# Optimization experiments

Hardware: AMD Instinct MI355X
Metric: run time of the kernel (lower is better)

The kernel has to match this reference:

```python
import jax, jax.numpy as jnp
import numpy as np

H = 16          # num_attention_heads
DH = 64         # attention_head_size
HID = H * DH    # hidden_size = 1024
EPS = 1e-12


def _layernorm(x, gamma, beta):
    mu = jnp.mean(x, axis=-1, keepdims=True)
    var = jnp.mean(jnp.square(x - mu), axis=-1, keepdims=True)
    return (x - mu) * jax.lax.rsqrt(var + EPS) * gamma + beta


def _attention(q, k, v, mask, Wo, bo, gamma, beta):
    # q,k,v: [B,S,HID] already linearly projected
    B, Tq, _ = q.shape
    Tk = k.shape[1]
    qh = q.reshape(B, Tq, H, DH)
    kh = k.reshape(B, Tk, H, DH)
    vh = v.reshape(B, Tk, H, DH)
    scores = jnp.einsum('bqhd,bkhd->bhqk', qh, kh) / np.sqrt(DH).astype(q.dtype)
    if mask is not None:
        scores = scores + mask  # mask broadcasts [B,1,1,Tk]
    probs = jax.nn.softmax(scores, axis=-1)
    ctx = jnp.einsum('bhqk,bkhd->bqhd', probs, vh)
    proj = jnp.einsum('bqhd,hdo->bqo', ctx, Wo) + bo
    # NOTE: residual is the projected query q (faithful to the source)
    return _layernorm(q + proj, gamma, beta)


def setup_inputs() -> dict:
    key = jax.random.key(0)
    ks = jax.random.split(key, 20)
    B, T, S = 4, 1024, 1024
    s = 0.02
    inp = {
        'encoder_states': jax.random.normal(ks[0], (B, S, HID), jnp.float32),
        'decoder_inputs': jax.random.normal(ks[1], (B, T, HID), jnp.float32),
        'src_attention_mask': jnp.zeros((B, 1, 1, S), jnp.float32),
        'tgt_attention_mask': jnp.zeros((B, 1, 1, T), jnp.float32),
        'Wq': jax.random.normal(ks[2], (HID, HID), jnp.float32) * s,
        'bq': jnp.zeros((HID,), jnp.float32),
        'Wk': jax.random.normal(ks[3], (HID, HID), jnp.float32) * s,
        'bk': jnp.zeros((HID,), jnp.float32),
        'Wv': jax.random.normal(ks[4], (HID, HID), jnp.float32) * s,
        'bv': jnp.zeros((HID,), jnp.float32),
        'Wq2': jax.random.normal(ks[5], (HID, HID), jnp.float32) * s,
        'bq2': jnp.zeros((HID,), jnp.float32),
        'Wk2': jax.random.normal(ks[6], (HID, HID), jnp.float32) * s,
        'bk2': jnp.zeros((HID,), jnp.float32),
        'Wv2': jax.random.normal(ks[7], (HID, HID), jnp.float32) * s,
        'bv2': jnp.zeros((HID,), jnp.float32),
        'Wo': jax.random.normal(ks[8], (H, DH, HID), jnp.float32) * s,
        'bo': jnp.zeros((HID,), jnp.float32),
        'gamma': jnp.ones((HID,), jnp.float32),
        'beta': jnp.zeros((HID,), jnp.float32),
    }
    return inp


def reference(encoder_states, decoder_inputs, src_attention_mask, tgt_attention_mask,
              Wq, bq, Wk, bk, Wv, bv, Wq2, bq2, Wk2, bk2, Wv2, bv2,
              Wo, bo, gamma, beta):
    # self-attention over decoder inputs
    q1 = decoder_inputs @ Wq + bq
    k1 = decoder_inputs @ Wk + bk
    v1 = decoder_inputs @ Wv + bv
    self_out = _attention(q1, k1, v1, tgt_attention_mask, Wo, bo, gamma, beta)
    # cross-attention: query from self_out, key/value from encoder states
    q2 = self_out @ Wq2 + bq2
    k2 = encoder_states @ Wk2 + bk2
    v2 = encoder_states @ Wv2 + bv2
    return _attention(q2, k2, v2, src_attention_mask, Wo, bo, gamma, beta)
```

## Files before the change

kernel.cpp:

```cpp
#include <hip/hip_runtime.h>
#include <stdint.h>


typedef unsigned short u16;
typedef __bf16 bf16x8 __attribute__((ext_vector_type(8)));
typedef float f32x4 __attribute__((ext_vector_type(4)));

#define AS1 __attribute__((address_space(1)))
#define AS3 __attribute__((address_space(3)))
typedef AS3 char lds_char;
typedef AS3 unsigned short lds_u16;

#define VMCNT(n) asm volatile("s_waitcnt vmcnt(" #n ")" ::: "memory")
#define LGKM0() asm volatile("s_waitcnt lgkmcnt(0)" ::: "memory")
#define SBARRIER() asm volatile("s_barrier" ::: "memory")

__device__ __forceinline__ u16 f2bf(float f) {
  union { float f; uint32_t u; } v; v.f = f;
  uint32_t u = v.u;
  return (u16)((u + 0x7fffu + ((u >> 16) & 1u)) >> 16);
}

__device__ __forceinline__ float bf2f(u16 b) {
  union { uint32_t u; float f; } v; v.u = ((uint32_t)b) << 16;
  return v.f;
}

__device__ __forceinline__ uint32_t cvt_pk_bf16(float lo, float hi) {
  uint32_t r;
  asm("v_cvt_pk_bf16_f32 %0, %1, %2" : "=v"(r) : "v"(lo), "v"(hi));
  return r;
}

__device__ __forceinline__ void gl_lds16(const void* g, void* l) {
  __builtin_amdgcn_global_load_lds((AS1 void*)(g), (AS3 void*)(l), 16, 0, 0);
}

__device__ __forceinline__ bf16x8 dsr128(const lds_u16* p) {
  bf16x8 r;
  asm volatile("ds_read_b128 %0, %1" : "=v"(r) : "v"(p));
  return r;
}

__device__ __forceinline__ int swz(int row, int byte) {
  return row * 128 + (byte ^ ((row & 7) << 4));
}

__global__ void __launch_bounds__(256)
convert2_kernel(const float* __restrict__ in0, u16* __restrict__ out0,
                const float* __restrict__ in1, u16* __restrict__ out1) {
  const int half = blockIdx.x >> 12;
  const int i = (blockIdx.x & 4095) * 256 + threadIdx.x;
  const float* in = half ? in1 : in0;
  u16* out = half ? out1 : out0;
  float4 v = ((const float4*)in)[i];
  ushort4 o;
  o.x = f2bf(v.x); o.y = f2bf(v.y); o.z = f2bf(v.z); o.w = f2bf(v.w);
  ((ushort4*)out)[i] = o;
}

struct WP { const float* w[7]; };

__global__ void __launch_bounds__(256)
transpose_kernel(WP wp, u16* __restrict__ out) {
  __shared__ float tile[64][65];
  const float* W = wp.w[blockIdx.z];
  u16* Wt = out + (size_t)blockIdx.z * 1024 * 1024;
  const int k0 = blockIdx.y * 64, n0 = blockIdx.x * 64;
  const int t = threadIdx.x;
  const int r = t >> 4, c4 = (t & 15) * 4;
#pragma unroll
  for (int rr = 0; rr < 64; rr += 16) {
    float4 v = *(const float4*)&W[(size_t)(k0 + r + rr) * 1024 + n0 + c4];
    tile[r + rr][c4 + 0] = v.x; tile[r + rr][c4 + 1] = v.y;
    tile[r + rr][c4 + 2] = v.z; tile[r + rr][c4 + 3] = v.w;
  }
  __syncthreads();
  const int n = t >> 2, seg = (t & 3) * 16;
  union { u16 s[16]; uint4 q[2]; } u;
#pragma unroll
  for (int i = 0; i < 16; ++i) u.s[i] = f2bf(tile[seg + i][n]);
  uint4* dst = (uint4*)&Wt[(size_t)(n0 + n) * 1024 + k0 + seg];
  dst[0] = u.q[0]; dst[1] = u.q[1];
}

__global__ void __launch_bounds__(512, 2)
qkv4c_kernel(const u16* __restrict__ A0, const u16* __restrict__ A1,
             const u16* __restrict__ A2, const u16* __restrict__ Bt,
             const float* __restrict__ b0, const float* __restrict__ b1,
             const float* __restrict__ b2,
             u16* __restrict__ qb, u16* __restrict__ kb, u16* __restrict__ vt) {
  __shared__ u16 SH[65536];

  const int d = blockIdx.y * 12 + blockIdx.x;
  const int c = d & 7, ci = d >> 3;
  const int mt = (c & 3) * 4 + (ci & 3);
  const int nt = (c >> 2) * 6 + (ci >> 2);
  const int bm = mt * 256, bn = nt * 256;
  const int seg = nt >> 2;
  const u16* A = (seg == 0) ? A0 : (seg == 1) ? A1 : A2;

  const int t = threadIdx.x, wv = t >> 6, ln = t & 63;
  const int wm = (wv >> 2) * 128, wn = (wv & 3) * 64;
  const int lcol = ln & 15, g = ln >> 4;
  const int aoff = (g * 16) ^ (((lcol >> 1) & 3) << 4);

  lds_char* ABase = (lds_char*)&SH[0];
  lds_char* BBase = (lds_char*)&SH[32768];

  const int st_row = wv * 16 + (ln >> 2);
  const int st_srcb = (((ln & 3) ^ ((ln >> 3) & 3)) * 16);
  auto stageA = [&](int buf, int k0) {
#pragma unroll
    for (int hf = 0; hf < 2; ++hf) {
      const int row = hf * 128 + st_row;
      gl_lds16((const char*)A + ((size_t)(bm + row) * 1024 + k0) * 2 + st_srcb,
               (char*)&SH[0] + buf * 16384 + hf * 8192 + wv * 1024);
    }
  };
  auto stageB = [&](int buf, int k0) {
#pragma unroll
    for (int hf = 0; hf < 2; ++hf) {
      const int row = hf * 128 + st_row;
      gl_lds16((const char*)Bt + ((size_t)(bn + row) * 1024 + k0) * 2 + st_srcb,
               (char*)&SH[32768] + buf * 16384 + hf * 8192 + wv * 1024);
    }
  };

  f32x4 acc[8][4] = {};

  stageA(0, 0); stageB(0, 0);
  stageA(1, 32); stageB(1, 32);
  stageA(2, 64); stageB(2, 64);
  VMCNT(8);
  __builtin_amdgcn_s_barrier();

  for (int kt = 0; kt < 32; ++kt) {
    const int buf = kt & 3;
    lds_char* Ab = ABase + buf * 16384;
    lds_char* Bb = BBase + buf * 16384;
    const int sbuf = (kt + 3) & 3;
    const int sk = (kt + 3) * 32;
    const bool do_st = kt < 29;
    bf16x8 afr[4], bfr[4];

#pragma unroll
    for (int j = 0; j < 4; ++j)
      bfr[j] = dsr128((const lds_u16*)(Bb + (wn + j * 16 + lcol) * 64 + aoff));
#pragma unroll
    for (int i = 0; i < 4; ++i)
      afr[i] = dsr128((const lds_u16*)(Ab + (wm + i * 16 + lcol) * 64 + aoff));
    if (do_st) stageA(sbuf, sk);
    __builtin_amdgcn_s_barrier();
    LGKM0();
    __builtin_amdgcn_sched_barrier(0);
    __builtin_amdgcn_s_setprio(1);
#pragma unroll
    for (int i = 0; i < 4; ++i)
#pragma unroll
      for (int j = 0; j < 4; ++j)
        acc[i][j] = __builtin_amdgcn_mfma_f32_16x16x32_bf16(afr[i], bfr[j], acc[i][j], 0, 0, 0);
    __builtin_amdgcn_s_setprio(0);
    __builtin_amdgcn_s_barrier();

#pragma unroll
    for (int i = 0; i < 4; ++i)
      afr[i] = dsr128((const lds_u16*)(Ab + (wm + 64 + i * 16 + lcol) * 64 + aoff));
    if (do_st) stageB(sbuf, sk);
    __builtin_amdgcn_s_barrier();
    LGKM0();
    __builtin_amdgcn_sched_barrier(0);
    __builtin_amdgcn_s_setprio(1);
#pragma unroll
    for (int i = 0; i < 4; ++i)
#pragma unroll
      for (int j = 0; j < 4; ++j)
        acc[4 + i][j] = __builtin_amdgcn_mfma_f32_16x16x32_bf16(afr[i], bfr[j], acc[4 + i][j], 0, 0, 0);
    __builtin_amdgcn_s_setprio(0);
    if (kt < 29)       { VMCNT(8); }
    else if (kt == 29) { VMCNT(4); }
    else if (kt == 30) { VMCNT(0); }
    __builtin_amdgcn_s_barrier();
  }

  const int cs = bn & 1023;
  const float* bias = (seg == 0) ? b0 : (seg == 1) ? b1 : b2;

  if (seg == 2) {
#pragma unroll
    for (int j = 0; j < 4; ++j) {
      const int col_l = wn + j * 16 + lcol;
      const float bc = bias[cs + col_l];
#pragma unroll
      for (int i = 0; i < 8; ++i) {
        const int m4 = wm + i * 16 + g * 4;
        ushort4 o;
        o.x = f2bf(acc[i][j][0] + bc); o.y = f2bf(acc[i][j][1] + bc);
        o.z = f2bf(acc[i][j][2] + bc); o.w = f2bf(acc[i][j][3] + bc);
        *(ushort4*)((char*)SH + col_l * 512 + ((m4 * 2) ^ ((col_l & 7) << 4))) = o;
      }
    }
  } else {
#pragma unroll
    for (int j = 0; j < 4; ++j) {
      const int col_l = wn + j * 16 + lcol;
      const float bc = bias[cs + col_l];
#pragma unroll
      for (int i = 0; i < 8; ++i) {
        const int m0 = wm + i * 16 + g * 4;
#pragma unroll
        for (int r = 0; r < 4; ++r)
          SH[(m0 + r) * 256 + (col_l ^ (((m0 + r) & 7) << 3))] = f2bf(acc[i][j][r] + bc);
      }
    }
  }
  __builtin_amdgcn_s_barrier();

  {
    const int R = t >> 1, hb = t & 1;
    u16* gp;
    if (seg == 2) {
      const int col = cs + R;
      const int h = col >> 6, dd = col & 63;
      gp = vt + ((size_t)((bm >> 10) * 16 + h) * 64 + dd) * 1024 + (bm & 1023) + hb * 128;
    } else {
      u16* outp = (seg == 0) ? qb : kb;
      gp = outp + (size_t)(bm + R) * 1024 + cs + hb * 128;
    }
#pragma unroll
    for (int cix = 0; cix < 16; ++cix) {
      uint4 v = *(uint4*)((char*)SH + R * 512 + ((hb * 256 + cix * 16) ^ ((R & 7) << 4)));
      *(uint4*)(gp + cix * 8) = v;
    }
  }
}

__global__ void __launch_bounds__(256)
gemm_proj(const u16* __restrict__ A, const u16* __restrict__ Bt,
          const float* __restrict__ bias, const u16* __restrict__ resid,
          float* __restrict__ outf) {
  __shared__ u16 Alds[2][8192];
  __shared__ u16 Blds[2][8192];
  const int d = blockIdx.y * 8 + blockIdx.x;
  const int c = d & 7, ci = d >> 3;
  const int mt = (c & 3) * 8 + (ci & 7);
  const int nt = (c >> 2) * 4 + (ci >> 3);
  const int bm = mt * 128, bn = nt * 128;
  const int t = threadIdx.x, wv = t >> 6, ln = t & 63;
  const int wm = (wv >> 1) * 64, wn = (wv & 1) * 64;
  const int lcol = ln & 15, lk8 = (ln >> 4) * 8, lr4 = (ln >> 4) * 4;

  f32x4 acc[4][4] = {};

  auto STAGE = [&](int buf, int k0) {
#pragma unroll
    for (int cc = 0; cc < 4; ++cc) {
      const int o = cc * 4096 + wv * 1024 + ln * 16;
      const int row = o >> 7, colb = o & 127;
      gl_lds16((const char*)A + ((size_t)(bm + row) * 1024 + k0) * 2 + colb,
               (char*)Alds[buf] + cc * 4096 + wv * 1024);
      gl_lds16((const char*)Bt + ((size_t)(bn + row) * 1024 + k0) * 2 + colb,
               (char*)Blds[buf] + cc * 4096 + wv * 1024);
    }
  };

  auto COMPUTE = [&](int buf) {
    const u16* Ab = Alds[buf];
    const u16* Bb = Blds[buf];
#pragma unroll
    for (int ks = 0; ks < 2; ++ks) {
      bf16x8 a[4], b[4];
#pragma unroll
      for (int i = 0; i < 4; ++i)
        a[i] = *(const bf16x8*)&Ab[(wm + i * 16 + lcol) * 64 + ks * 32 + lk8];
#pragma unroll
      for (int j = 0; j < 4; ++j)
        b[j] = *(const bf16x8*)&Bb[(wn + j * 16 + lcol) * 64 + ks * 32 + lk8];
#pragma unroll
      for (int i = 0; i < 4; ++i)
#pragma unroll
        for (int j = 0; j < 4; ++j)
          acc[i][j] = __builtin_amdgcn_mfma_f32_16x16x32_bf16(a[i], b[j], acc[i][j], 0, 0, 0);
    }
  };

  STAGE(0, 0);
  int cur = 0;
  for (int it = 0; it < 15; ++it) {
    STAGE(cur ^ 1, (it + 1) * 64);
    VMCNT(8);
    SBARRIER();
    COMPUTE(cur);
    SBARRIER();
    cur ^= 1;
  }
  VMCNT(0);
  SBARRIER();
  COMPUTE(cur);

#pragma unroll
  for (int j = 0; j < 4; ++j) {
    const int col = bn + wn + j * 16 + lcol;
    const float bc = bias[col];
#pragma unroll
    for (int i = 0; i < 4; ++i) {
      const int row0 = bm + wm + i * 16 + lr4;
#pragma unroll
      for (int r = 0; r < 4; ++r) {
        const size_t idx = (size_t)(row0 + r) * 1024 + col;
        outf[idx] = acc[i][j][r] + bc + bf2f(resid[idx]);
      }
    }
  }
}

__global__ void __launch_bounds__(256)
attn_kernel(const u16* __restrict__ Q, const u16* __restrict__ Kb,
            const u16* __restrict__ Vt, const float* __restrict__ mask,
            u16* __restrict__ ctx) {
  __shared__ u16 Klds[2][64 * 64];
  __shared__ u16 Vlds[2][64 * 64];
  __shared__ u16 Plds[4][16 * 64];

  const int fid = blockIdx.x;
  const int xcd = fid & 7, idx = fid >> 3;
  const int bh = xcd * 8 + (idx >> 4);
  const int b = bh >> 4, h = bh & 15;
  const int q0 = (idx & 15) * 64;

  const int t = threadIdx.x, wv = t >> 6, ln = t & 63;
  const int lcol = ln & 15, g = ln >> 4;
  const int lk8 = g * 8, c0 = g * 16;

  const int qrow = q0 + wv * 16 + lcol;
  const u16* qptr = Q + ((size_t)(b * 1024 + qrow) * 1024 + h * 64);
  bf16x8 qa[2];
  qa[0] = *(const bf16x8*)(qptr + lk8);
  qa[1] = *(const bf16x8*)(qptr + 32 + lk8);

  const float* mrow = mask + b * 1024;
  char* pbase = (char*)&Plds[wv][0];

  f32x4 accO[4] = {};
  float m_r = -1e30f, l_r = 0.f;

  auto STAGE = [&](int buf, int s0) {
#pragma unroll
    for (int c = 0; c < 2; ++c) {
      const int o = c * 4096 + wv * 1024 + ln * 16;
      const int row = o >> 7;
      const int src_cb = (o & 127) ^ ((row & 7) << 4);
      gl_lds16((const char*)Kb + ((size_t)((b * 1024 + s0 + row) * 1024 + h * 64)) * 2 + src_cb,
               (char*)Klds[buf] + c * 4096 + wv * 1024);
      gl_lds16((const char*)Vt + ((size_t)(((b * 16 + h) * 64 + row) * 1024 + s0)) * 2 + src_cb,
               (char*)Vlds[buf] + c * 4096 + wv * 1024);
    }
  };

  auto TILE = [&](int buf, const float4* mk) {
    f32x4 accST[4] = {};
    __builtin_amdgcn_s_setprio(1);
#pragma unroll
    for (int ks = 0; ks < 2; ++ks)
#pragma unroll
      for (int sb = 0; sb < 4; ++sb) {
        bf16x8 kb = *(const bf16x8*)((const char*)Klds[buf] + swz(sb * 16 + lcol, ks * 64 + c0));
        accST[sb] = __builtin_amdgcn_mfma_f32_16x16x32_bf16(kb, qa[ks], accST[sb], 0, 0, 0);
      }
    __builtin_amdgcn_s_setprio(0);

    float sv[4][4];
#pragma unroll
    for (int sb = 0; sb < 4; ++sb) {
      sv[sb][0] = accST[sb][0] * 0.125f + mk[sb].x;
      sv[sb][1] = accST[sb][1] * 0.125f + mk[sb].y;
      sv[sb][2] = accST[sb][2] * 0.125f + mk[sb].z;
      sv[sb][3] = accST[sb][3] * 0.125f + mk[sb].w;
    }
    float mt = sv[0][0];
#pragma unroll
    for (int sb = 0; sb < 4; ++sb)
#pragma unroll
      for (int r = 0; r < 4; ++r) mt = fmaxf(mt, sv[sb][r]);
    mt = fmaxf(mt, __shfl_xor(mt, 16));
    mt = fmaxf(mt, __shfl_xor(mt, 32));

    const bool nr = __all(mt <= m_r + 8.0f) != 0;
    float alpha = 1.0f;
    if (!nr) {
      const float mn2 = fmaxf(m_r, mt);
      alpha = __expf(m_r - mn2);
      m_r = mn2;
    }
    float rs = 0.f;
#pragma unroll
    for (int sb = 0; sb < 4; ++sb)
#pragma unroll
      for (int r = 0; r < 4; ++r) {
        const float pp = __expf(sv[sb][r] - m_r);
        sv[sb][r] = pp;
        rs += pp;
      }
    rs += __shfl_xor(rs, 16);
    rs += __shfl_xor(rs, 32);
    l_r = nr ? (l_r + rs) : (l_r * alpha + rs);

#pragma unroll
    for (int sb = 0; sb < 4; ++sb) {
      uint2 dd;
      dd.x = cvt_pk_bf16(sv[sb][0], sv[sb][1]);
      dd.y = cvt_pk_bf16(sv[sb][2], sv[sb][3]);
      *(uint2*)(pbase + swz(lcol, sb * 32 + g * 8)) = dd;
    }

    if (!nr) {
#pragma unroll
      for (int df = 0; df < 4; ++df)
#pragma unroll
        for (int r = 0; r < 4; ++r) accO[df][r] *= alpha;
    }
    __builtin_amdgcn_s_setprio(1);
#pragma unroll
    for (int ks = 0; ks < 2; ++ks) {
      bf16x8 pb = *(const bf16x8*)(pbase + swz(lcol, ks * 64 + c0));
#pragma unroll
      for (int df = 0; df < 4; ++df) {
        bf16x8 va = *(const bf16x8*)((const char*)Vlds[buf] + swz(df * 16 + lcol, ks * 64 + c0));
        accO[df] = __builtin_amdgcn_mfma_f32_16x16x32_bf16(va, pb, accO[df], 0, 0, 0);
      }
    }
    __builtin_amdgcn_s_setprio(0);
  };

  STAGE(0, 0);
  float4 mk_cur[4];
#pragma unroll
  for (int sb = 0; sb < 4; ++sb)
    mk_cur[sb] = *(const float4*)&mrow[sb * 16 + g * 4];

  int cur = 0;
  for (int ti = 0; ti < 15; ++ti) {
    const int s1 = ti * 64 + 64;
    STAGE(cur ^ 1, s1);
    float4 mk_nxt[4];
#pragma unroll
    for (int sb = 0; sb < 4; ++sb)
      mk_nxt[sb] = *(const float4*)&mrow[s1 + sb * 16 + g * 4];
    VMCNT(12);
    SBARRIER();
    TILE(cur, mk_cur);
    SBARRIER();
#pragma unroll
    for (int sb = 0; sb < 4; ++sb) mk_cur[sb] = mk_nxt[sb];
    cur ^= 1;
  }
  VMCNT(4);
  SBARRIER();
  TILE(cur, mk_cur);

  const float inv = 1.0f / l_r;
  u16* cp = ctx + ((size_t)(b * 1024 + qrow) * 1024 + h * 64);
#pragma unroll
  for (int df = 0; df < 4; ++df) {
    ushort4 o;
    o.x = f2bf(accO[df][0] * inv); o.y = f2bf(accO[df][1] * inv);
    o.z = f2bf(accO[df][2] * inv); o.w = f2bf(accO[df][3] * inv);
    *(ushort4*)(cp + df * 16 + g * 4) = o;
  }
}

template <int OUTF>
__global__ void __launch_bounds__(256)
ln_kernel(const float* __restrict__ x, const float* __restrict__ gamma,
          const float* __restrict__ beta, float* __restrict__ outf,
          u16* __restrict__ outb) {
  const int row = blockIdx.x, t = threadIdx.x;
  const float* xr = x + (size_t)row * 1024;
  float4 v = *(const float4*)&xr[t * 4];
  float s = v.x + v.y + v.z + v.w;
  float q = v.x * v.x + v.y * v.y + v.z * v.z + v.w * v.w;
#pragma unroll
  for (int off = 1; off < 64; off <<= 1) {
    s += __shfl_xor(s, off);
    q += __shfl_xor(q, off);
  }
  __shared__ float ws[4], wq[4];
  if ((t & 63) == 0) { ws[t >> 6] = s; wq[t >> 6] = q; }
  __syncthreads();
  s = ws[0] + ws[1] + ws[2] + ws[3];
  q = wq[0] + wq[1] + wq[2] + wq[3];
  const float mu = s * (1.0f / 1024.0f);
  float var = q * (1.0f / 1024.0f) - mu * mu;
  var = fmaxf(var, 0.0f);
  const float rstd = rsqrtf(var + 1e-12f);
  float4 g = *(const float4*)&gamma[t * 4];
  float4 be = *(const float4*)&beta[t * 4];
  float y0 = (v.x - mu) * rstd * g.x + be.x;
  float y1 = (v.y - mu) * rstd * g.y + be.y;
  float y2 = (v.z - mu) * rstd * g.z + be.z;
  float y3 = (v.w - mu) * rstd * g.w + be.w;
  if constexpr (OUTF) {
    float4 o; o.x = y0; o.y = y1; o.z = y2; o.w = y3;
    *(float4*)&outf[(size_t)row * 1024 + t * 4] = o;
  } else {
    ushort4 o; o.x = f2bf(y0); o.y = f2bf(y1); o.z = f2bf(y2); o.w = f2bf(y3);
    *(ushort4*)&outb[(size_t)row * 1024 + t * 4] = o;
  }
}

extern "C" void kernel_launch(void* const* d_in, const int* in_sizes, int n_in,
                              void* d_out, int out_size, void* d_ws, size_t ws_size,
                              hipStream_t stream) {
  const float* enc = (const float*)d_in[0];
  const float* dec = (const float*)d_in[1];
  const float* src_mask = (const float*)d_in[2];
  const float* tgt_mask = (const float*)d_in[3];
  const float* Wq  = (const float*)d_in[4];  const float* bq  = (const float*)d_in[5];
  const float* Wk  = (const float*)d_in[6];  const float* bk  = (const float*)d_in[7];
  const float* Wv  = (const float*)d_in[8];  const float* bv  = (const float*)d_in[9];
  const float* Wq2 = (const float*)d_in[10]; const float* bq2 = (const float*)d_in[11];
  const float* Wk2 = (const float*)d_in[12]; const float* bk2 = (const float*)d_in[13];
  const float* Wv2 = (const float*)d_in[14]; const float* bv2 = (const float*)d_in[15];
  const float* Wo  = (const float*)d_in[16]; const float* bo  = (const float*)d_in[17];
  const float* gamma = (const float*)d_in[18]; const float* beta = (const float*)d_in[19];
  float* out = (float*)d_out;

  char* p = (char*)d_ws;
  const size_t ABF = (size_t)4096 * 1024 * 2;
  const size_t AF  = (size_t)4096 * 1024 * 4;
  const size_t WBF = (size_t)1024 * 1024 * 2;
  u16* decbf = (u16*)p; p += ABF;
  u16* encbf = (u16*)p; p += ABF;
  u16* wt    = (u16*)p; p += 7 * WBF;
  u16* qbf   = (u16*)p; p += ABF;
  u16* kbf   = (u16*)p; p += ABF;
  u16* vtb   = (u16*)p; p += ABF;
  u16* ctxb  = (u16*)p; p += ABF;
  float* tmpf = (float*)p; p += AF;
  u16* sobf  = decbf;

  u16* WoT  = wt + 6 * 1048576;

  dim3 b256(256);
  convert2_kernel<<<8192, b256, 0, stream>>>(dec, decbf, enc, encbf);
  WP wp;
  wp.w[0] = Wq; wp.w[1] = Wk; wp.w[2] = Wv; wp.w[3] = Wq2;
  wp.w[4] = Wk2; wp.w[5] = Wv2; wp.w[6] = Wo;
  transpose_kernel<<<dim3(16, 16, 7), b256, 0, stream>>>(wp, wt);

  qkv4c_kernel<<<dim3(12, 16), 512, 0, stream>>>(
      decbf, decbf, decbf, wt, bq, bk, bv, qbf, kbf, vtb);
  attn_kernel<<<1024, b256, 0, stream>>>(qbf, kbf, vtb, tgt_mask, ctxb);
  gemm_proj<<<dim3(8, 32), b256, 0, stream>>>(ctxb, WoT, bo, qbf, tmpf);
  ln_kernel<0><<<4096, b256, 0, stream>>>(tmpf, gamma, beta, nullptr, sobf);
  qkv4c_kernel<<<dim3(12, 16), 512, 0, stream>>>(
      sobf, encbf, encbf, wt + 3 * 1048576, bq2, bk2, bv2, qbf, kbf, vtb);
  attn_kernel<<<1024, b256, 0, stream>>>(qbf, kbf, vtb, src_mask, ctxb);
  gemm_proj<<<dim3(8, 32), b256, 0, stream>>>(ctxb, WoT, bo, qbf, tmpf);
  ln_kernel<1><<<4096, b256, 0, stream>>>(tmpf, gamma, beta, out, nullptr);
}
```

Before: 233.9 us.

## Shrink QKV GEMM tiles to 256x128 and triple-buffer swizzled projection GEMM

The fused QKV GEMM moves from 256x256 tiles with four LDS buffers to 256x128 tiles with three buffers, smaller LDS and a higher occupancy hint. The grid doubles to 384 blocks to fill more CUs. The output projection GEMM gets a three-stage pipeline with XOR-swizzled LDS layout, full 64-wide K per iteration and priority hints, aiming to cut bank conflicts and hide load latency. Smaller tiles lower data reuse per block and add global traffic in exchange for better parallelism.

```diff
diff --git a/kernel.cpp b/kernel.cpp
--- a/kernel.cpp
+++ b/kernel.cpp
@@ -84,73 +84,62 @@
   dst[0] = u.q[0]; dst[1] = u.q[1];
 }
 
-__global__ void __launch_bounds__(512, 2)
-qkv4c_kernel(const u16* __restrict__ A0, const u16* __restrict__ A1,
+__global__ void __launch_bounds__(512, 4)
+qkv3b_kernel(const u16* __restrict__ A0, const u16* __restrict__ A1,
              const u16* __restrict__ A2, const u16* __restrict__ Bt,
              const float* __restrict__ b0, const float* __restrict__ b1,
              const float* __restrict__ b2,
              u16* __restrict__ qb, u16* __restrict__ kb, u16* __restrict__ vt) {
-  __shared__ u16 SH[65536];
-
-  const int d = blockIdx.y * 12 + blockIdx.x;
+  __shared__ u16 SH[36864];
+
+  const int d = blockIdx.y * 24 + blockIdx.x;
   const int c = d & 7, ci = d >> 3;
-  const int mt = (c & 3) * 4 + (ci & 3);
-  const int nt = (c >> 2) * 6 + (ci >> 2);
-  const int bm = mt * 256, bn = nt * 256;
-  const int seg = nt >> 2;
+  const int mt = ci & 15, nt = c * 3 + (ci >> 4);
+  const int bm = mt * 256, bn = nt * 128;
+  const int seg = nt >> 3;
+  const int cs = (nt & 7) * 128;
   const u16* A = (seg == 0) ? A0 : (seg == 1) ? A1 : A2;
 
   const int t = threadIdx.x, wv = t >> 6, ln = t & 63;
-  const int wm = (wv >> 2) * 128, wn = (wv & 3) * 64;
+  const int wm = (wv >> 1) * 64, wn = (wv & 1) * 64;
   const int lcol = ln & 15, g = ln >> 4;
   const int aoff = (g * 16) ^ (((lcol >> 1) & 3) << 4);
 
-  lds_char* ABase = (lds_char*)&SH[0];
-  lds_char* BBase = (lds_char*)&SH[32768];
-
-  const int st_row = wv * 16 + (ln >> 2);
-  const int st_srcb = (((ln & 3) ^ ((ln >> 3) & 3)) * 16);
-  auto stageA = [&](int buf, int k0) {
-#pragma unroll
-    for (int hf = 0; hf < 2; ++hf) {
-      const int row = hf * 128 + st_row;
+  lds_char* base = (lds_char*)&SH[0];
+  const int st_srcb = (((t & 3) ^ ((t >> 3) & 3)) * 16);
+  auto STAGE = [&](int buf, int k0) {
+#pragma unroll
+    for (int l = 0; l < 2; ++l) {
+      const int row = l * 128 + (t >> 2);
       gl_lds16((const char*)A + ((size_t)(bm + row) * 1024 + k0) * 2 + st_srcb,
-               (char*)&SH[0] + buf * 16384 + hf * 8192 + wv * 1024);
+               (char*)base + buf * 24576 + l * 8192 + (t >> 6) * 1024);
+    }
+    {
+      const int row = t >> 2;
+      gl_lds16((const char*)Bt + ((size_t)(bn + row) * 1024 + k0) * 2 + st_srcb,
+               (char*)base + buf * 24576 + 16384 + (t >> 6) * 1024);
     }
   };
-  auto stageB = [&](int buf, int k0) {
-#pragma unroll
-    for (int hf = 0; hf < 2; ++hf) {
-      const int row = hf * 128 + st_row;
-      gl_lds16((const char*)Bt + ((size_t)(bn + row) * 1024 + k0) * 2 + st_srcb,
-               (char*)&SH[32768] + buf * 16384 + hf * 8192 + wv * 1024);
-    }
-  };
-
-  f32x4 acc[8][4] = {};
-
-  stageA(0, 0); stageB(0, 0);
-  stageA(1, 32); stageB(1, 32);
-  stageA(2, 64); stageB(2, 64);
-  VMCNT(8);
+
+  f32x4 acc[4][4] = {};
+
+  STAGE(0, 0);
+  STAGE(1, 32);
+  VMCNT(3);
   __builtin_amdgcn_s_barrier();
 
+  int cur = 0, st = 2;
   for (int kt = 0; kt < 32; ++kt) {
-    const int buf = kt & 3;
-    lds_char* Ab = ABase + buf * 16384;
-    lds_char* Bb = BBase + buf * 16384;
-    const int sbuf = (kt + 3) & 3;
-    const int sk = (kt + 3) * 32;
-    const bool do_st = kt < 29;
+    lds_char* Ab = base + cur * 24576;
+    lds_char* Bb = Ab + 16384;
     bf16x8 afr[4], bfr[4];
-
 #pragma unroll
     for (int j = 0; j < 4; ++j)
       bfr[j] = dsr128((const lds_u16*)(Bb + (wn + j * 16 + lcol) * 64 + aoff));
 #pragma unroll
     for (int i = 0; i < 4; ++i)
       afr[i] = dsr128((const lds_u16*)(Ab + (wm + i * 16 + lcol) * 64 + aoff));
-    if (do_st) stageA(sbuf, sk);
+    if (kt < 30) STAGE(st, (kt + 2) * 32);
     __builtin_amdgcn_s_barrier();
     LGKM0();
     __builtin_amdgcn_sched_barrier(0);
@@ -161,29 +150,13 @@
       for (int j = 0; j < 4; ++j)
         acc[i][j] = __builtin_amdgcn_mfma_f32_16x16x32_bf16(afr[i], bfr[j], acc[i][j], 0, 0, 0);
     __builtin_amdgcn_s_setprio(0);
-    __builtin_amdgcn_s_barrier();
-
-#pragma unroll
-    for (int i = 0; i < 4; ++i)
-      afr[i] = dsr128((const lds_u16*)(Ab + (wm + 64 + i * 16 + lcol) * 64 + aoff));
-    if (do_st) stageB(sbuf, sk);
-    __builtin_amdgcn_s_barrier();
-    LGKM0();
-    __builtin_amdgcn_sched_barrier(0);
-    __builtin_amdgcn_s_setprio(1);
-#pragma unroll
-    for (int i = 0; i < 4; ++i)
-#pragma unroll
-      for (int j = 0; j < 4; ++j)
-        acc[4 + i][j] = __builtin_amdgcn_mfma_f32_16x16x32_bf16(afr[i], bfr[j], acc[4 + i][j], 0, 0, 0);
-    __builtin_amdgcn_s_setprio(0);
-    if (kt < 29)       { VMCNT(8); }
-    else if (kt == 29) { VMCNT(4); }
+    if (kt < 30)       { VMCNT(3); }
     else if (kt == 30) { VMCNT(0); }
     __builtin_amdgcn_s_barrier();
-  }
-
-  const int cs = bn & 1023;
+    cur = (cur == 2) ? 0 : cur + 1;
+    st  = (st == 2)  ? 0 : st + 1;
+  }
+
   const float* bias = (seg == 0) ? b0 : (seg == 1) ? b1 : b2;
 
   if (seg == 2) {
@@ -192,7 +165,7 @@
       const int col_l = wn + j * 16 + lcol;
       const float bc = bias[cs + col_l];
 #pragma unroll
-      for (int i = 0; i < 8; ++i) {
+      for (int i = 0; i < 4; ++i) {
         const int m4 = wm + i * 16 + g * 4;
         ushort4 o;
         o.x = f2bf(acc[i][j][0] + bc); o.y = f2bf(acc[i][j][1] + bc);
@@ -206,30 +179,33 @@
       const int col_l = wn + j * 16 + lcol;
       const float bc = bias[cs + col_l];
 #pragma unroll
-      for (int i = 0; i < 8; ++i) {
+      for (int i = 0; i < 4; ++i) {
         const int m0 = wm + i * 16 + g * 4;
 #pragma unroll
         for (int r = 0; r < 4; ++r)
-          SH[(m0 + r) * 256 + (col_l ^ (((m0 + r) & 7) << 3))] = f2bf(acc[i][j][r] + bc);
+          SH[(m0 + r) * 128 + (col_l ^ (((m0 + r) & 7) << 3))] = f2bf(acc[i][j][r] + bc);
       }
     }
   }
   __builtin_amdgcn_s_barrier();
 
-  {
+  if (seg == 2) {
+    const int C = t >> 2, q = t & 3;
+    const int col = cs + C;
+    const int h = col >> 6, dd = col & 63;
+    u16* gp = vt + ((size_t)((bm >> 10) * 16 + h) * 64 + dd) * 1024 + (bm & 1023) + q * 64;
+#pragma unroll
+    for (int cix = 0; cix < 8; ++cix) {
+      uint4 v = *(uint4*)((char*)SH + C * 512 + ((q * 128 + cix * 16) ^ ((C & 7) << 4)));
+      *(uint4*)(gp + cix * 8) = v;
+    }
+  } else {
     const int R = t >> 1, hb = t & 1;
-    u16* gp;
-    if (seg == 2) {
-      const int col = cs + R;
-      const int h = col >> 6, dd = col & 63;
-      gp = vt + ((size_t)((bm >> 10) * 16 + h) * 64 + dd) * 1024 + (bm & 1023) + hb * 128;
-    } else {
-      u16* outp = (seg == 0) ? qb : kb;
-      gp = outp + (size_t)(bm + R) * 1024 + cs + hb * 128;
-    }
-#pragma unroll
-    for (int cix = 0; cix < 16; ++cix) {
-      uint4 v = *(uint4*)((char*)SH + R * 512 + ((hb * 256 + cix * 16) ^ ((R & 7) << 4)));
+    u16* outp = (seg == 0) ? qb : kb;
+    u16* gp = outp + (size_t)(bm + R) * 1024 + cs + hb * 64;
+#pragma unroll
+    for (int cix = 0; cix < 8; ++cix) {
+      uint4 v = *(uint4*)((char*)SH + R * 256 + ((hb * 128 + cix * 16) ^ ((R & 7) << 4)));
       *(uint4*)(gp + cix * 8) = v;
     }
   }
@@ -239,8 +215,8 @@
 gemm_proj(const u16* __restrict__ A, const u16* __restrict__ Bt,
           const float* __restrict__ bias, const u16* __restrict__ resid,
           float* __restrict__ outf) {
-  __shared__ u16 Alds[2][8192];
-  __shared__ u16 Blds[2][8192];
+  __shared__ u16 Alds[3][8192];
+  __shared__ u16 Blds[3][8192];
   const int d = blockIdx.y * 8 + blockIdx.x;
   const int c = d & 7, ci = d >> 3;
   const int mt = (c & 3) * 8 + (ci & 7);
@@ -248,55 +224,67 @@
   const int bm = mt * 128, bn = nt * 128;
   const int t = threadIdx.x, wv = t >> 6, ln = t & 63;
   const int wm = (wv >> 1) * 64, wn = (wv & 1) * 64;
-  const int lcol = ln & 15, lk8 = (ln >> 4) * 8, lr4 = (ln >> 4) * 4;
+  const int lcol = ln & 15, g = ln >> 4, lr4 = g * 4;
+  const int xr = (lcol & 7) << 4;
+  const int aoff0 = (g * 16) ^ xr;
+  const int aoff1 = (64 + g * 16) ^ xr;
 
   f32x4 acc[4][4] = {};
 
+  const int st_srcb = (((t & 7) ^ ((t >> 3) & 7)) * 16);
   auto STAGE = [&](int buf, int k0) {
 #pragma unroll
-    for (int cc = 0; cc < 4; ++cc) {
-      const int o = cc * 4096 + wv * 1024 + ln * 16;
-      const int row = o >> 7, colb = o & 127;
-      gl_lds16((const char*)A + ((size_t)(bm + row) * 1024 + k0) * 2 + colb,
-               (char*)Alds[buf] + cc * 4096 + wv * 1024);
-      gl_lds16((const char*)Bt + ((size_t)(bn + row) * 1024 + k0) * 2 + colb,
-               (char*)Blds[buf] + cc * 4096 + wv * 1024);
+    for (int l = 0; l < 4; ++l) {
+      const int row = l * 32 + (t >> 3);
+      gl_lds16((const char*)A + ((size_t)(bm + row) * 1024 + k0) * 2 + st_srcb,
+               (char*)&Alds[buf][0] + l * 4096 + (t >> 6) * 1024);
+      gl_lds16((const char*)Bt + ((size_t)(bn + row) * 1024 + k0) * 2 + st_srcb,
+               (char*)&Blds[buf][0] + l * 4096 + (t >> 6) * 1024);
     }
   };
 
-  auto COMPUTE = [&](int buf) {
-    const u16* Ab = Alds[buf];
-    const u16* Bb = Blds[buf];
-#pragma unroll
-    for (int ks = 0; ks < 2; ++ks) {
-      bf16x8 a[4], b[4];
-#pragma unroll
-      for (int i = 0; i < 4; ++i)
-        a[i] = *(const bf16x8*)&Ab[(wm + i * 16 + lcol) * 64 + ks * 32 + lk8];
+  STAGE(0, 0);
+  STAGE(1, 64);
+  VMCNT(8);
+  __builtin_amdgcn_s_barrier();
+
+  int cur = 0, st = 2;
+  for (int it = 0; it < 16; ++it) {
+    lds_char* Ab = (lds_char*)&Alds[cur][0];
+    lds_char* Bb = (lds_char*)&Blds[cur][0];
+    bf16x8 a0[4], b0v[4], a1[4], b1v[4];
+#pragma unroll
+    for (int i = 0; i < 4; ++i) {
+      a0[i]  = dsr128((const lds_u16*)(Ab + (wm + i * 16 + lcol) * 128 + aoff0));
+      b0v[i] = dsr128((const lds_u16*)(Bb + (wn + i * 16 + lcol) * 128 + aoff0));
+    }
+#pragma unroll
+    for (int i = 0; i < 4; ++i) {
+      a1[i]  = dsr128((const lds_u16*)(Ab + (wm + i * 16 + lcol) * 128 + aoff1));
+      b1v[i] = dsr128((const lds_u16*)(Bb + (wn + i * 16 + lcol) * 128 + aoff1));
+    }
+    if (it < 14) STAGE(st, (it + 2) * 64);
+    __builtin_amdgcn_s_barrier();
+    LGKM0();
+    __builtin_amdgcn_sched_barrier(0);
+    __builtin_amdgcn_s_setprio(1);
+#pragma unroll
+    for (int i = 0; i < 4; ++i)
 #pragma unroll
       for (int j = 0; j < 4; ++j)
-        b[j] = *(const bf16x8*)&Bb[(wn + j * 16 + lcol) * 64 + ks * 32 + lk8];
-#pragma unroll
-      for (int i = 0; i < 4; ++i)
-#pragma unroll
-        for (int j = 0; j < 4; ++j)
-          acc[i][j] = __builtin_amdgcn_mfma_f32_16x16x32_bf16(a[i], b[j], acc[i][j], 0, 0, 0);
-    }
-  };
-
-  STAGE(0, 0);
-  int cur = 0;
-  for (int it = 0; it < 15; ++it) {
-    STAGE(cur ^ 1, (it + 1) * 64);
-    VMCNT(8);
-    SBARRIER();
-    COMPUTE(cur);
-    SBARRIER();
-    cur ^= 1;
-  }
-  VMCNT(0);
-  SBARRIER();
-  COMPUTE(cur);
+        acc[i][j] = __builtin_amdgcn_mfma_f32_16x16x32_bf16(a0[i], b0v[j], acc[i][j], 0, 0, 0);
+#pragma unroll
+    for (int i = 0; i < 4; ++i)
+#pragma unroll
+      for (int j = 0; j < 4; ++j)
+        acc[i][j] = __builtin_amdgcn_mfma_f32_16x16x32_bf16(a1[i], b1v[j], acc[i][j], 0, 0, 0);
+    __builtin_amdgcn_s_setprio(0);
+    if (it < 14)       { VMCNT(8); }
+    else if (it == 14) { VMCNT(0); }
+    __builtin_amdgcn_s_barrier();
+    cur = (cur == 2) ? 0 : cur + 1;
+    st  = (st == 2)  ? 0 : st + 1;
+  }
 
 #pragma unroll
   for (int j = 0; j < 4; ++j) {
@@ -548,12 +536,12 @@
   wp.w[4] = Wk2; wp.w[5] = Wv2; wp.w[6] = Wo;
   transpose_kernel<<<dim3(16, 16, 7), b256, 0, stream>>>(wp, wt);
 
-  qkv4c_kernel<<<dim3(12, 16), 512, 0, stream>>>(
+  qkv3b_kernel<<<dim3(24, 16), 512, 0, stream>>>(
       decbf, decbf, decbf, wt, bq, bk, bv, qbf, kbf, vtb);
   attn_kernel<<<1024, b256, 0, stream>>>(qbf, kbf, vtb, tgt_mask, ctxb);
   gemm_proj<<<dim3(8, 32), b256, 0, stream>>>(ctxb, WoT, bo, qbf, tmpf);
   ln_kernel<0><<<4096, b256, 0, stream>>>(tmpf, gamma, beta, nullptr, sobf);
-  qkv4c_kernel<<<dim3(12, 16), 512, 0, stream>>>(
+  qkv3b_kernel<<<dim3(24, 16), 512, 0, stream>>>(
       sobf, encbf, encbf, wt + 3 * 1048576, bq2, bk2, bv2, qbf, kbf, vtb);
   attn_kernel<<<1024, b256, 0, stream>>>(qbf, kbf, vtb, src_mask, ctxb);
   gemm_proj<<<dim3(8, 32), b256, 0, stream>>>(ctxb, WoT, bo, qbf, tmpf);
```

Result: faster. 218.9 us, median of 2 (-6.4%).
